# Performance work log

Hardware: AMD Instinct MI355X
Metric: run time of the kernel (lower is better)

The kernel has to match this reference:

```python
import jax, jax.numpy as jnp
import numpy as np
from jax import lax

B_, T_, C_ = 8, 1024, 768
H_, W_ = 32, 32
N_LAYER, LAYER_ID = 12, 5


def _fancy_init():
    # faithful 'fancy' init from Random_SpatialMix._init_weights
    r01 = LAYER_ID / (N_LAYER - 1)
    r1a0 = 1.0 - LAYER_ID / N_LAYER
    h = np.arange(C_, dtype=np.float64)
    decay = -5 + 8 * (h / (C_ - 1)) ** (0.7 + 1.3 * r01)
    zig = ((np.arange(C_) + 1) % 3 - 1) * 0.5
    first = np.log(0.3) + zig
    xlin = h / C_
    mix_k = xlin ** r1a0
    mix_v = xlin ** r1a0 + 0.3 * r01
    mix_r = xlin ** (0.5 * r1a0)
    f32 = lambda a: jnp.asarray(a, jnp.float32)
    return f32(decay), f32(first), f32(mix_k), f32(mix_v), f32(mix_r)


def setup_inputs() -> dict:
    key = jax.random.key(0)
    ks = jax.random.split(key, 6)
    s = 1.0 / np.sqrt(C_)
    x = jax.random.normal(ks[0], (B_, T_, C_), jnp.float32)
    Wk = jax.random.normal(ks[1], (C_, C_), jnp.float32) * s
    Wv = jax.random.normal(ks[2], (C_, C_), jnp.float32) * s
    Wr = jax.random.normal(ks[3], (C_, C_), jnp.float32) * s
    Wo = jax.random.normal(ks[4], (C_, C_), jnp.float32) * s
    decay, first, mk, mv, mr = _fancy_init()
    perm = jax.random.permutation(ks[5], C_).astype(jnp.int32)
    return dict(x=x, w_key=Wk, w_value=Wv, w_receptance=Wr, w_output=Wo,
                spatial_decay=decay, spatial_first=first,
                mix_k=mk, mix_v=mv, mix_r=mr, perm=perm, H=H_, W=W_)


def _shift2d(a, dh, dw, H, W):
    # zero-padded 2D shift of [B,H,W,g]
    pad = [(0, 0), (max(dh, 0), max(-dh, 0)), (max(dw, 0), max(-dw, 0)), (0, 0)]
    a = jnp.pad(a, pad)
    return a[:, max(-dh, 0):max(-dh, 0) + H, max(-dw, 0):max(-dw, 0) + W, :]


def q_shift(x, H, W, shift_pixel=1, gamma=0.25):
    # VRWKV q_shift: 4 channel groups shifted right/left/down/up, rest copied
    B, T, C = x.shape
    xi = x.reshape(B, H, W, C)
    g = int(C * gamma)
    parts = [
        _shift2d(xi[..., 0:g], 0, shift_pixel, H, W),
        _shift2d(xi[..., g:2 * g], 0, -shift_pixel, H, W),
        _shift2d(xi[..., 2 * g:3 * g], shift_pixel, 0, H, W),
        _shift2d(xi[..., 3 * g:4 * g], -shift_pixel, 0, H, W),
        xi[..., 4 * g:],
    ]
    return jnp.concatenate(parts, axis=-1).reshape(B, T, C)


def wkv(w, u, k, v):
    # RWKV-v4 WKV kernel (numerically stable form). w,u: [C]; k,v: [B,T,C]
    w = -jnp.exp(w)  # kernel applies w = -exp(w)
    B, T, C = k.shape

    def step(carry, kv):
        a, b, p = carry  # each [B,C]
        kt, vt = kv
        q = jnp.maximum(p, u + kt)
        e1 = jnp.exp(p - q)
        e2 = jnp.exp(u + kt - q)
        y = (e1 * a + e2 * vt) / (e1 * b + e2)
        q2 = jnp.maximum(p + w, kt)
        e1 = jnp.exp(p + w - q2)
        e2 = jnp.exp(kt - q2)
        return (e1 * a + e2 * vt, e1 * b + e2, q2), y

    init = (jnp.zeros((B, C), k.dtype), jnp.zeros((B, C), k.dtype),
            jnp.full((B, C), -1e38, k.dtype))
    _, y = lax.scan(step, init, (jnp.moveaxis(k, 1, 0), jnp.moveaxis(v, 1, 0)))
    return jnp.moveaxis(y, 0, 1)


def reference(x, w_key, w_value, w_receptance, w_output,
              spatial_decay, spatial_first, mix_k, mix_v, mix_r, perm, H, W):
    B, T, C = x.shape
    xx = q_shift(x, H, W)
    xk = x * mix_k + xx * (1 - mix_k)
    xv = x * mix_v + xx * (1 - mix_v)
    xr = x * mix_r + xx * (1 - mix_r)
    k = xk @ w_key.T
    v = xv @ w_value.T
    sr = jax.nn.sigmoid(xr @ w_receptance.T)
    # training path: shuffle CHANNEL axis (RevShuffle dim=2), run WKV, reverse
    ks_ = k[:, :, perm]
    vs_ = v[:, :, perm]
    wkv_s = wkv(spatial_decay / T, spatial_first / T, ks_, vs_)
    rev = jnp.zeros_like(perm).at[perm].set(jnp.arange(C, dtype=perm.dtype))
    wkv_out = wkv_s[:, :, rev]
    return (sr * wkv_out) @ w_output.T
```

## Files before the change

kernel.cpp:

```cpp
#include <hip/hip_runtime.h>
#include <hip/hip_bf16.h>
#include <stdint.h>

#define B_N 8
#define T_N 1024
#define C_N 768
#define M_N (B_N*T_N)
#define NCH 32
#define LCH (T_N/NCH)
#define BK  64

typedef __attribute__((ext_vector_type(4))) float f32x4;
typedef __attribute__((ext_vector_type(8))) short s16x8;
typedef __attribute__((ext_vector_type(4))) unsigned short u16x4;

__device__ __forceinline__ unsigned short f2bf(float f){
  unsigned int u = __float_as_uint(f);
  u += 0x7FFFu + ((u >> 16) & 1u);
  return (unsigned short)(u >> 16);
}
__device__ __forceinline__ float bf2f(unsigned short h){
  return __uint_as_float(((unsigned int)h) << 16);
}

__device__ __forceinline__ void async16(const unsigned short* g, unsigned short* l){
  __builtin_amdgcn_global_load_lds(
      (const __attribute__((address_space(1))) unsigned int*)g,
      (__attribute__((address_space(3))) unsigned int*)l, 16, 0, 0);
}

__global__ __launch_bounds__(256) void prep_weights(
    const float* __restrict__ Wk, const float* __restrict__ Wv,
    const float* __restrict__ Wr, const float* __restrict__ Wo,
    const int* __restrict__ perm,
    unsigned short* __restrict__ Wall,
    unsigned short* __restrict__ Wop)
{
  int idx = blockIdx.x*256 + threadIdx.x;
  int r = idx / C_N, c = idx - r*C_N;
  int pr = perm[r];
  Wall[idx]            = f2bf(Wk[pr*C_N + c]);
  Wall[idx +   (size_t)C_N*C_N] = f2bf(Wv[pr*C_N + c]);
  Wall[idx + 2*(size_t)C_N*C_N] = f2bf(Wr[pr*C_N + c]);
  Wop[idx] = f2bf(Wo[r*C_N + perm[c]]);
}

__global__ __launch_bounds__(256) void mix_kernel(
    const float* __restrict__ x,
    const float* __restrict__ mk, const float* __restrict__ mv, const float* __restrict__ mr,
    unsigned short* __restrict__ xk, unsigned short* __restrict__ xv, unsigned short* __restrict__ xr)
{
  int idx = blockIdx.x*256 + threadIdx.x;
  int n  = idx / (C_N/4);
  int c4 = (idx - n*(C_N/4)) * 4;
  int t = n & (T_N-1);
  int h = t >> 5, w = t & 31;
  int grp = c4 / 192;
  int dh = (grp==2) ? -1 : (grp==3) ? 1 : 0;
  int dw = (grp==0) ? -1 : (grp==1) ? 1 : 0;
  int h2 = h + dh, w2 = w + dw;
  bool valid = ((unsigned)h2 < 32u) && ((unsigned)w2 < 32u);
  f32x4 xc = *(const f32x4*)(x + (size_t)n*C_N + c4);
  f32x4 xx = {0.f,0.f,0.f,0.f};
  if (valid) xx = *(const f32x4*)(x + (size_t)(n + dh*32 + dw)*C_N + c4);
  f32x4 vk = *(const f32x4*)(mk + c4);
  f32x4 vv = *(const f32x4*)(mv + c4);
  f32x4 vr = *(const f32x4*)(mr + c4);
  u16x4 ok, ov, orr;
  #pragma unroll
  for (int i=0;i<4;++i){
    float d = xc[i] - xx[i];
    ok[i]  = f2bf(xx[i] + vk[i]*d);
    ov[i]  = f2bf(xx[i] + vv[i]*d);
    orr[i] = f2bf(xx[i] + vr[i]*d);
  }
  *(u16x4*)(xk + (size_t)n*C_N + c4) = ok;
  *(u16x4*)(xv + (size_t)n*C_N + c4) = ov;
  *(u16x4*)(xr + (size_t)n*C_N + c4) = orr;
}

__global__ __launch_bounds__(256) void gemm_kvr(
    const unsigned short* __restrict__ xk, const unsigned short* __restrict__ xv,
    const unsigned short* __restrict__ xr,
    const unsigned short* __restrict__ Wall,
    float* __restrict__ kp, float* __restrict__ vp, unsigned short* __restrict__ srb)
{
  const int m0 = blockIdx.x*128, n0 = blockIdx.y*128;
  const int z  = blockIdx.y / 6;
  const unsigned short* A = (z==0)? xk : (z==1)? xv : xr;
  __shared__ __align__(16) unsigned short As[2][128*BK];
  __shared__ __align__(16) unsigned short Bs[2][128*BK];
  const int tid = threadIdx.x;
  const int lane = tid & 63, wid = tid >> 6;
  const int wr = wid >> 1, wc = wid & 1;
  f32x4 acc[4][4];
  #pragma unroll
  for (int i=0;i<4;++i)
    #pragma unroll
    for (int j=0;j<4;++j) acc[i][j] = (f32x4){0.f,0.f,0.f,0.f};

  const int srow = tid >> 3;
  const int scol = (((tid & 7) ^ ((tid >> 3) & 7)) * 8);
  const int lr  = lane & 15;
  const int x7  = lr & 7;
  const int kh  = lane >> 4;

  auto stage = [&](int buf, int k0){
    #pragma unroll
    for (int it=0; it<4; ++it){
      int r = it*32 + srow;
      async16(&A   [(size_t)(m0+r)*C_N + k0 + scol], &As[buf][(it*32 + wid*8)*BK]);
      async16(&Wall[(size_t)(n0+r)*C_N + k0 + scol], &Bs[buf][(it*32 + wid*8)*BK]);
    }
  };

  stage(0, 0);
  __syncthreads();
  int cur = 0;
  for (int k0 = 0; k0 < C_N; k0 += BK){
    if (k0 + BK < C_N) stage(cur^1, k0 + BK);
    #pragma unroll
    for (int kk=0; kk<BK; kk+=32){
      const int g = (kk>>3) + kh;
      const int pg = (g ^ x7) << 3;
      s16x8 af[4], bfr[4];
      #pragma unroll
      for (int mi=0;mi<4;++mi) af[mi]  = *(const s16x8*)&As[cur][(wr*64 + mi*16 + lr)*BK + pg];
      #pragma unroll
      for (int ni=0;ni<4;++ni) bfr[ni] = *(const s16x8*)&Bs[cur][(wc*64 + ni*16 + lr)*BK + pg];
      #pragma unroll
      for (int mi=0;mi<4;++mi)
        #pragma unroll
        for (int ni=0;ni<4;++ni)
          acc[mi][ni] = __builtin_amdgcn_mfma_f32_16x16x32_bf16(af[mi], bfr[ni], acc[mi][ni], 0,0,0);
    }
    __syncthreads();
    cur ^= 1;
  }
  const int lr4 = (lane>>4)*4, lc = lane & 15;
  const int colbase = n0 - z*C_N;
  #pragma unroll
  for (int mi=0;mi<4;++mi){
    #pragma unroll
    for (int ni=0;ni<4;++ni){
      #pragma unroll
      for (int i=0;i<4;++i){
        int m = m0 + wr*64 + mi*16 + lr4 + i;
        int n = colbase + wc*64 + ni*16 + lc;
        float val = acc[mi][ni][i];
        if (z==0)      kp[(size_t)m*C_N + n] = val;
        else if (z==1) vp[(size_t)m*C_N + n] = val;
        else           srb[(size_t)m*C_N + n] = f2bf(1.f/(1.f + __expf(-val)));
      }
    }
  }
}

__global__ __launch_bounds__(256) void gemm_out(
    const unsigned short* __restrict__ A, const unsigned short* __restrict__ Bw,
    float* __restrict__ out)
{
  const int m0 = blockIdx.x*128, n0 = blockIdx.y*128;
  __shared__ __align__(16) unsigned short As[2][128*BK];
  __shared__ __align__(16) unsigned short Bs[2][128*BK];
  const int tid = threadIdx.x;
  const int lane = tid & 63, wid = tid >> 6;
  const int wr = wid >> 1, wc = wid & 1;
  f32x4 acc[4][4];
  #pragma unroll
  for (int i=0;i<4;++i)
    #pragma unroll
    for (int j=0;j<4;++j) acc[i][j] = (f32x4){0.f,0.f,0.f,0.f};

  const int srow = tid >> 3;
  const int scol = (((tid & 7) ^ ((tid >> 3) & 7)) * 8);
  const int lr  = lane & 15;
  const int x7  = lr & 7;
  const int kh  = lane >> 4;

  auto stage = [&](int buf, int k0){
    #pragma unroll
    for (int it=0; it<4; ++it){
      int r = it*32 + srow;
      async16(&A [(size_t)(m0+r)*C_N + k0 + scol], &As[buf][(it*32 + wid*8)*BK]);
      async16(&Bw[(size_t)(n0+r)*C_N + k0 + scol], &Bs[buf][(it*32 + wid*8)*BK]);
    }
  };

  stage(0, 0);
  __syncthreads();
  int cur = 0;
  for (int k0 = 0; k0 < C_N; k0 += BK){
    if (k0 + BK < C_N) stage(cur^1, k0 + BK);
    #pragma unroll
    for (int kk=0; kk<BK; kk+=32){
      const int g = (kk>>3) + kh;
      const int pg = (g ^ x7) << 3;
      s16x8 af[4], bfr[4];
      #pragma unroll
      for (int mi=0;mi<4;++mi) af[mi]  = *(const s16x8*)&As[cur][(wr*64 + mi*16 + lr)*BK + pg];
      #pragma unroll
      for (int ni=0;ni<4;++ni) bfr[ni] = *(const s16x8*)&Bs[cur][(wc*64 + ni*16 + lr)*BK + pg];
      #pragma unroll
      for (int mi=0;mi<4;++mi)
        #pragma unroll
        for (int ni=0;ni<4;++ni)
          acc[mi][ni] = __builtin_amdgcn_mfma_f32_16x16x32_bf16(af[mi], bfr[ni], acc[mi][ni], 0,0,0);
    }
    __syncthreads();
    cur ^= 1;
  }
  const int lr4 = (lane>>4)*4, lc = lane & 15;
  #pragma unroll
  for (int mi=0;mi<4;++mi)
    #pragma unroll
    for (int ni=0;ni<4;++ni)
      #pragma unroll
      for (int i=0;i<4;++i){
        int m = m0 + wr*64 + mi*16 + lr4 + i;
        int n = n0 + wc*64 + ni*16 + lc;
        out[(size_t)m*C_N + n] = acc[mi][ni][i];
      }
}

__global__ __launch_bounds__(256) void wkv_phase1(
    const float* __restrict__ kp, const float* __restrict__ vp,
    const float* __restrict__ decay,
    float* __restrict__ sa, float* __restrict__ sb, float* __restrict__ sp)
{
  int g = blockIdx.x*256 + threadIdx.x;
  int j = g % C_N;
  int cb = g / C_N;
  int b = cb % B_N, c = cb / B_N;
  float w = -__expf(decay[j] * (1.0f/T_N));
  float a = 0.f, bb = 0.f, p = -1e38f;
  size_t base = ((size_t)b*T_N + c*LCH)*C_N + j;
  #pragma unroll 4
  for (int t = 0; t < LCH; ++t){
    size_t o = base + (size_t)t*C_N;
    float kt = kp[o], vt = vp[o];
    float pw = p + w;
    float q2 = fmaxf(pw, kt);
    float e1 = __expf(pw - q2), e2 = __expf(kt - q2);
    a  = e1*a + e2*vt;
    bb = e1*bb + e2;
    p  = q2;
  }
  sa[g] = a; sb[g] = bb; sp[g] = p;
}

__global__ __launch_bounds__(256) void wkv_phase2(
    const float* __restrict__ decay,
    float* __restrict__ sa, float* __restrict__ sb, float* __restrict__ sp)
{
  int g = blockIdx.x*256 + threadIdx.x;
  int j = g % C_N, b = g / C_N;
  float w = -__expf(decay[j] * (1.0f/T_N));
  float wL = w * (float)LCH;
  float a = 0.f, bb = 0.f, p = -1e38f;
  for (int c = 0; c < NCH; ++c){
    size_t idx = ((size_t)c*B_N + b)*C_N + j;
    float la = sa[idx], lb = sb[idx], lp = sp[idx];
    sa[idx] = a; sb[idx] = bb; sp[idx] = p;
    float p1 = p + wL;
    float pn = fmaxf(p1, lp);
    float e1 = __expf(p1 - pn), e2 = __expf(lp - pn);
    a  = e1*a + e2*la;
    bb = e1*bb + e2*lb;
    p  = pn;
  }
}

__global__ __launch_bounds__(256) void wkv_phase3(
    const float* __restrict__ kp, const float* __restrict__ vp,
    const unsigned short* __restrict__ srb,
    const float* __restrict__ decay, const float* __restrict__ first,
    const float* __restrict__ sa, const float* __restrict__ sb,
    const float* __restrict__ sp,
    unsigned short* __restrict__ zp)
{
  int g = blockIdx.x*256 + threadIdx.x;
  int j = g % C_N;
  int cb = g / C_N;
  int b = cb % B_N, c = cb / B_N;
  float w = -__expf(decay[j] * (1.0f/T_N));
  float u = first[j] * (1.0f/T_N);
  float a = sa[g], bb = sb[g], p = sp[g];
  size_t base = ((size_t)b*T_N + c*LCH)*C_N + j;
  #pragma unroll 2
  for (int t = 0; t < LCH; ++t){
    size_t o = base + (size_t)t*C_N;
    float kt = kp[o], vt = vp[o];
    float uk = u + kt;
    float q  = fmaxf(p, uk);
    float e1 = __expf(p - q), e2 = __expf(uk - q);
    float y  = __fdividef(e1*a + e2*vt, e1*bb + e2);
    zp[o] = f2bf(bf2f(srb[o]) * y);
    float pw = p + w;
    float q2 = fmaxf(pw, kt);
    float e1b = __expf(pw - q2), e2b = __expf(kt - q2);
    a  = e1b*a + e2b*vt;
    bb = e1b*bb + e2b;
    p  = q2;
  }
}

extern "C" void kernel_launch(void* const* d_in, const int* in_sizes, int n_in,
                              void* d_out, int out_size, void* d_ws, size_t ws_size,
                              hipStream_t stream)
{
  const float* x     = (const float*)d_in[0];
  const float* Wk    = (const float*)d_in[1];
  const float* Wv    = (const float*)d_in[2];
  const float* Wr    = (const float*)d_in[3];
  const float* Wo    = (const float*)d_in[4];
  const float* decay = (const float*)d_in[5];
  const float* first = (const float*)d_in[6];
  const float* mk    = (const float*)d_in[7];
  const float* mv    = (const float*)d_in[8];
  const float* mr    = (const float*)d_in[9];
  const int*   perm  = (const int*)d_in[10];
  float* out = (float*)d_out;

  char* ws = (char*)d_ws;
  size_t off = 0;
  auto alloc = [&](size_t bytes)->char* {
    char* p = ws + off;
    off += (bytes + 255) & ~(size_t)255;
    return p;
  };
  const size_t MC = (size_t)M_N * C_N;
  const size_t CC = (size_t)C_N * C_N;
  const size_t SC = (size_t)NCH * B_N * C_N;
  unsigned short* xk   = (unsigned short*)alloc(MC*2);
  unsigned short* xv   = (unsigned short*)alloc(MC*2);
  unsigned short* xr   = (unsigned short*)alloc(MC*2);
  unsigned short* zp   = (unsigned short*)alloc(MC*2);
  unsigned short* Wall = (unsigned short*)alloc(CC*3*2);
  unsigned short* Wop  = (unsigned short*)alloc(CC*2);
  unsigned short* srb  = (unsigned short*)alloc(MC*2);
  float* kp  = (float*)alloc(MC*4);
  float* vp  = (float*)alloc(MC*4);
  float* sa  = (float*)alloc(SC*4);
  float* sb  = (float*)alloc(SC*4);
  float* sp  = (float*)alloc(SC*4);

  prep_weights<<<dim3(CC/256), dim3(256), 0, stream>>>(Wk, Wv, Wr, Wo, perm,
                                                       Wall, Wop);
  mix_kernel<<<dim3(MC/4/256), dim3(256), 0, stream>>>(x, mk, mv, mr, xk, xv, xr);
  gemm_kvr<<<dim3(M_N/128, 3*C_N/128), dim3(256), 0, stream>>>(
      xk, xv, xr, Wall, kp, vp, srb);
  wkv_phase1<<<dim3(SC/256), dim3(256), 0, stream>>>(kp, vp, decay, sa, sb, sp);
  wkv_phase2<<<dim3(B_N*C_N/256), dim3(256), 0, stream>>>(decay, sa, sb, sp);
  wkv_phase3<<<dim3(SC/256), dim3(256), 0, stream>>>(kp, vp, srb, decay, first,
                                                     sa, sb, sp, zp);
  gemm_out<<<dim3(M_N/128, C_N/128), dim3(256), 0, stream>>>(zp, Wop, out);
}
```

Before: 125.6 us.

## Enlarge KVR GEMM tiles to 256x256 with swizzled blocks and finer-grained pipeline sync

The fused K/V/R projection GEMM moves from 128x128 tiles with 4 waves to 256x256 tiles with 8 waves (each wave 128x64), and the block index is swizzled so consecutive blocks share N tiles. Both GEMMs replace __syncthreads with an explicit vmcnt wait plus raw barriers so the next stage's loads stay in flight during compute, and they raise wave priority around the MFMA bursts. The aim is more operand reuse per LDS load, fewer redundant global reads and better overlap of loads with compute. In exchange it uses 128KB of LDS per block and many more accumulator registers, which lowers occupancy, and the grid drops to 288 blocks.

```diff
diff --git a/kernel.cpp b/kernel.cpp
--- a/kernel.cpp
+++ b/kernel.cpp
@@ -9,6 +9,7 @@
 #define NCH 32
 #define LCH (T_N/NCH)
 #define BK  64
+#define KT  (C_N/BK)
 
 typedef __attribute__((ext_vector_type(4))) float f32x4;
 typedef __attribute__((ext_vector_type(8))) short s16x8;
@@ -79,23 +80,28 @@
   *(u16x4*)(xr + (size_t)n*C_N + c4) = orr;
 }
 
-__global__ __launch_bounds__(256) void gemm_kvr(
+__global__ __launch_bounds__(512) void gemm_kvr(
     const unsigned short* __restrict__ xk, const unsigned short* __restrict__ xv,
     const unsigned short* __restrict__ xr,
     const unsigned short* __restrict__ Wall,
     float* __restrict__ kp, float* __restrict__ vp, unsigned short* __restrict__ srb)
 {
-  const int m0 = blockIdx.x*128, n0 = blockIdx.y*128;
-  const int z  = blockIdx.y / 6;
+  int flat = blockIdx.y * gridDim.x + blockIdx.x;
+  int swz  = (flat & 7) * 36 + (flat >> 3);
+  const int m0 = (swz & 31) * 256;
+  const int nb = swz >> 5;
+  const int n0 = nb * 256;
+  const int z  = nb / 3;
   const unsigned short* A = (z==0)? xk : (z==1)? xv : xr;
-  __shared__ __align__(16) unsigned short As[2][128*BK];
-  __shared__ __align__(16) unsigned short Bs[2][128*BK];
+
+  __shared__ __align__(16) unsigned short As[2][256*BK];
+  __shared__ __align__(16) unsigned short Bs[2][256*BK];
   const int tid = threadIdx.x;
   const int lane = tid & 63, wid = tid >> 6;
-  const int wr = wid >> 1, wc = wid & 1;
-  f32x4 acc[4][4];
-  #pragma unroll
-  for (int i=0;i<4;++i)
+  const int wr = wid >> 2, wc = wid & 3;
+  f32x4 acc[8][4];
+  #pragma unroll
+  for (int i=0;i<8;++i)
     #pragma unroll
     for (int j=0;j<4;++j) acc[i][j] = (f32x4){0.f,0.f,0.f,0.f};
 
@@ -108,44 +114,56 @@
   auto stage = [&](int buf, int k0){
     #pragma unroll
     for (int it=0; it<4; ++it){
-      int r = it*32 + srow;
-      async16(&A   [(size_t)(m0+r)*C_N + k0 + scol], &As[buf][(it*32 + wid*8)*BK]);
-      async16(&Wall[(size_t)(n0+r)*C_N + k0 + scol], &Bs[buf][(it*32 + wid*8)*BK]);
-    }
-  };
-
-  stage(0, 0);
-  __syncthreads();
-  int cur = 0;
-  for (int k0 = 0; k0 < C_N; k0 += BK){
-    if (k0 + BK < C_N) stage(cur^1, k0 + BK);
+      int r = it*64 + srow;
+      async16(&A   [(size_t)(m0+r)*C_N + k0 + scol], &As[buf][(it*64 + wid*8)*BK]);
+      async16(&Wall[(size_t)(n0+r)*C_N + k0 + scol], &Bs[buf][(it*64 + wid*8)*BK]);
+    }
+  };
+
+  auto compute = [&](int buf){
     #pragma unroll
     for (int kk=0; kk<BK; kk+=32){
       const int g = (kk>>3) + kh;
       const int pg = (g ^ x7) << 3;
-      s16x8 af[4], bfr[4];
-      #pragma unroll
-      for (int mi=0;mi<4;++mi) af[mi]  = *(const s16x8*)&As[cur][(wr*64 + mi*16 + lr)*BK + pg];
-      #pragma unroll
-      for (int ni=0;ni<4;++ni) bfr[ni] = *(const s16x8*)&Bs[cur][(wc*64 + ni*16 + lr)*BK + pg];
-      #pragma unroll
-      for (int mi=0;mi<4;++mi)
+      s16x8 af[8], bfr[4];
+      #pragma unroll
+      for (int mi=0;mi<8;++mi) af[mi]  = *(const s16x8*)&As[buf][(wr*128 + mi*16 + lr)*BK + pg];
+      #pragma unroll
+      for (int ni=0;ni<4;++ni) bfr[ni] = *(const s16x8*)&Bs[buf][(wc*64 + ni*16 + lr)*BK + pg];
+      __builtin_amdgcn_s_setprio(1);
+      #pragma unroll
+      for (int mi=0;mi<8;++mi)
         #pragma unroll
         for (int ni=0;ni<4;++ni)
           acc[mi][ni] = __builtin_amdgcn_mfma_f32_16x16x32_bf16(af[mi], bfr[ni], acc[mi][ni], 0,0,0);
-    }
-    __syncthreads();
+      __builtin_amdgcn_s_setprio(0);
+    }
+  };
+
+  stage(0, 0);
+  int cur = 0;
+  #pragma unroll 1
+  for (int t = 0; t < KT-1; ++t){
+    stage(cur^1, (t+1)*BK);
+    asm volatile("s_waitcnt vmcnt(8)" ::: "memory");
+    __builtin_amdgcn_s_barrier();
+    compute(cur);
+    __builtin_amdgcn_s_barrier();
     cur ^= 1;
   }
+  asm volatile("s_waitcnt vmcnt(0)" ::: "memory");
+  __builtin_amdgcn_s_barrier();
+  compute(cur);
+
   const int lr4 = (lane>>4)*4, lc = lane & 15;
   const int colbase = n0 - z*C_N;
   #pragma unroll
-  for (int mi=0;mi<4;++mi){
+  for (int mi=0;mi<8;++mi){
     #pragma unroll
     for (int ni=0;ni<4;++ni){
       #pragma unroll
       for (int i=0;i<4;++i){
-        int m = m0 + wr*64 + mi*16 + lr4 + i;
+        int m = m0 + wr*128 + mi*16 + lr4 + i;
         int n = colbase + wc*64 + ni*16 + lc;
         float val = acc[mi][ni][i];
         if (z==0)      kp[(size_t)m*C_N + n] = val;
@@ -187,29 +205,41 @@
     }
   };
 
-  stage(0, 0);
-  __syncthreads();
-  int cur = 0;
-  for (int k0 = 0; k0 < C_N; k0 += BK){
-    if (k0 + BK < C_N) stage(cur^1, k0 + BK);
+  auto compute = [&](int buf){
     #pragma unroll
     for (int kk=0; kk<BK; kk+=32){
       const int g = (kk>>3) + kh;
       const int pg = (g ^ x7) << 3;
       s16x8 af[4], bfr[4];
       #pragma unroll
-      for (int mi=0;mi<4;++mi) af[mi]  = *(const s16x8*)&As[cur][(wr*64 + mi*16 + lr)*BK + pg];
-      #pragma unroll
-      for (int ni=0;ni<4;++ni) bfr[ni] = *(const s16x8*)&Bs[cur][(wc*64 + ni*16 + lr)*BK + pg];
+      for (int mi=0;mi<4;++mi) af[mi]  = *(const s16x8*)&As[buf][(wr*64 + mi*16 + lr)*BK + pg];
+      #pragma unroll
+      for (int ni=0;ni<4;++ni) bfr[ni] = *(const s16x8*)&Bs[buf][(wc*64 + ni*16 + lr)*BK + pg];
+      __builtin_amdgcn_s_setprio(1);
       #pragma unroll
       for (int mi=0;mi<4;++mi)
         #pragma unroll
         for (int ni=0;ni<4;++ni)
           acc[mi][ni] = __builtin_amdgcn_mfma_f32_16x16x32_bf16(af[mi], bfr[ni], acc[mi][ni], 0,0,0);
-    }
-    __syncthreads();
+      __builtin_amdgcn_s_setprio(0);
+    }
+  };
+
+  stage(0, 0);
+  int cur = 0;
+  #pragma unroll 1
+  for (int t = 0; t < KT-1; ++t){
+    stage(cur^1, (t+1)*BK);
+    asm volatile("s_waitcnt vmcnt(8)" ::: "memory");
+    __builtin_amdgcn_s_barrier();
+    compute(cur);
+    __builtin_amdgcn_s_barrier();
     cur ^= 1;
   }
+  asm volatile("s_waitcnt vmcnt(0)" ::: "memory");
+  __builtin_amdgcn_s_barrier();
+  compute(cur);
+
   const int lr4 = (lane>>4)*4, lc = lane & 15;
   #pragma unroll
   for (int mi=0;mi<4;++mi)
@@ -348,7 +378,7 @@
   prep_weights<<<dim3(CC/256), dim3(256), 0, stream>>>(Wk, Wv, Wr, Wo, perm,
                                                        Wall, Wop);
   mix_kernel<<<dim3(MC/4/256), dim3(256), 0, stream>>>(x, mk, mv, mr, xk, xv, xr);
-  gemm_kvr<<<dim3(M_N/128, 3*C_N/128), dim3(256), 0, stream>>>(
+  gemm_kvr<<<dim3(M_N/256, 3*C_N/256), dim3(512), 0, stream>>>(
       xk, xv, xr, Wall, kp, vp, srb);
   wkv_phase1<<<dim3(SC/256), dim3(256), 0, stream>>>(kp, vp, decay, sa, sb, sp);
   wkv_phase2<<<dim3(B_N*C_N/256), dim3(256), 0, stream>>>(decay, sa, sb, sp);
```

Measured after the change: 142.4 us. 13.4% more time.
